# Performance work log

Hardware: AMD Instinct MI355X
Metric: run time of the kernel (lower is better)

The kernel has to match this reference:

```python
import jax, jax.numpy as jnp
import numpy as np

OFR = 2.0      # offset_range_factor
WSIZE = 8      # window_size
SPLIT = 1      # split_size


def _grid_sample(img, grid):
    # torch.nn.functional.grid_sample: bilinear, align_corners=True, padding_mode='zeros'
    # img: (B,C,H,W); grid: (B,Gh,Gw,2) with (x,y) in [-1,1]
    B, C, H, W = img.shape
    gx = (grid[..., 0] + 1.0) * 0.5 * (W - 1)
    gy = (grid[..., 1] + 1.0) * 0.5 * (H - 1)
    x0 = jnp.floor(gx)
    y0 = jnp.floor(gy)
    wx1 = gx - x0
    wy1 = gy - y0
    imgf = img.reshape(B, C, H * W)

    def corner(yc, xc, wgt):
        valid = (xc >= 0) & (xc <= W - 1) & (yc >= 0) & (yc <= H - 1)
        idx = (jnp.clip(yc, 0, H - 1) * W + jnp.clip(xc, 0, W - 1)).astype(jnp.int32)
        g = jnp.take_along_axis(imgf, idx.reshape(B, 1, -1), axis=2)  # (B,C,N)
        return g * (wgt * valid).reshape(B, 1, -1)

    out = (corner(y0, x0, (1 - wy1) * (1 - wx1)) + corner(y0, x0 + 1, (1 - wy1) * wx1)
           + corner(y0 + 1, x0, wy1 * (1 - wx1)) + corner(y0 + 1, x0 + 1, wy1 * wx1))
    return out.reshape(B, C, *grid.shape[1:-1])


def _win_attn(xqv, dh, dw):
    # 'b (qv c) (h dh) (w dw) -> qv (b h w) (dh dw) c' ; dot attention ; inverse rearrange
    B, cc, H, W = xqv.shape
    c = cc // 2
    t = xqv.reshape(B, 2, c, H // dh, dh, W // dw, dw)
    t = t.transpose(1, 0, 3, 5, 4, 6, 2).reshape(2, -1, dh * dw, c)
    q, v = t[0], t[1]
    atn = jax.nn.softmax(q @ jnp.swapaxes(q, -1, -2), axis=-1)
    o = atn @ v  # (nw, dh*dw, c)
    o = o.reshape(B, H // dh, W // dw, dh, dw, c).transpose(0, 5, 1, 3, 2, 4).reshape(B, c, H, W)
    return o


def setup_inputs() -> dict:
    key = jax.random.key(0)
    ks = jax.random.split(key, 16)
    C, B, H, W = 48, 2, 64, 64
    rn = lambda k, s, sc=0.05: (jax.random.normal(k, s) * sc).astype(jnp.float32)
    return {
        'x': jax.random.normal(ks[0], (B, C, H, W), jnp.float32),
        'Wq': rn(ks[1], (C, C)), 'bq': rn(ks[2], (C,)),
        'off_dw_w': rn(ks[3], (C, 1, 3, 3)), 'off_dw_b': rn(ks[4], (C,)),
        'off_ln_g': jnp.ones((C,), jnp.float32), 'off_ln_b': jnp.zeros((C,), jnp.float32),
        'off_pw_w': rn(ks[5], (2, C)),
        'Wk': rn(ks[6], (C, C)), 'bk': rn(ks[7], (C,)),
        'Wv': rn(ks[8], (C, C)), 'bv': rn(ks[9], (C,)),
        'inp_w': rn(ks[10], (2 * C, C)), 'inp_b': rn(ks[11], (2 * C,)),
        'bn_g': jnp.ones((2 * C,), jnp.float32), 'bn_b': jnp.zeros((2 * C,), jnp.float32),
        'bn_mean': jnp.zeros((2 * C,), jnp.float32), 'bn_var': jnp.ones((2 * C,), jnp.float32),
        'pout_w': rn(ks[12], (C, C)), 'pout_b': rn(ks[13], (C,)),
        'rpe': rn(ks[14], (1, 191, 191), 0.01),  # 96*2-1
    }


def reference(x, Wq, bq, off_dw_w, off_dw_b, off_ln_g, off_ln_b, off_pw_w, Wk, bk, Wv, bv,
              inp_w, inp_b, bn_g, bn_b, bn_mean, bn_var, pout_w, pout_b, rpe):
    B, C, h, w = x.shape
    scale = C ** (-0.5)
    c1 = lambda t, W_, b_=None: jnp.einsum('oc,bchw->bohw', W_, t) + (0.0 if b_ is None else b_[None, :, None, None])
    q = c1(x, Wq, bq)
    # conv_offset: depthwise 3x3 -> LayerNorm over channels -> GELU -> 1x1 to 2 ch (no bias)
    t = jax.lax.conv_general_dilated(q, off_dw_w, (1, 1), ((1, 1), (1, 1)),
                                     dimension_numbers=('NCHW', 'OIHW', 'NCHW'),
                                     feature_group_count=C) + off_dw_b[None, :, None, None]
    mu = t.mean(1, keepdims=True)
    var = ((t - mu) ** 2).mean(1, keepdims=True)
    t = (t - mu) * jax.lax.rsqrt(var + 1e-5) * off_ln_g[None, :, None, None] + off_ln_b[None, :, None, None]
    t = jax.nn.gelu(t, approximate=False)
    offset = c1(t, off_pw_w)  # (B,2,h,w), channel 0 = y, 1 = x
    n = h * w
    orange = jnp.array([1.0 / (h - 1), 1.0 / (w - 1)], jnp.float32).reshape(1, 2, 1, 1)
    offset = jnp.tanh(offset) * orange * OFR
    offset = offset.transpose(0, 2, 3, 1)  # (B,h,w,2) (y,x)
    ry = jnp.linspace(0.5, h - 0.5, h) / (h - 1) * 2.0 - 1.0
    rx = jnp.linspace(0.5, w - 0.5, w) / (w - 1) * 2.0 - 1.0
    ref = jnp.stack(jnp.meshgrid(ry, rx, indexing='ij'), -1)[None]
    pos = offset + ref  # (B,h,w,2) (y,x)
    x_sampled = _grid_sample(x, pos[..., ::-1]).reshape(B, C, n)
    # project_inp: 1x1 conv -> BatchNorm2d (eval mode)
    x2 = c1(x, inp_w, inp_b)
    x2 = (x2 - bn_mean[None, :, None, None]) * jax.lax.rsqrt(bn_var + 1e-5)[None, :, None, None] \
         * bn_g[None, :, None, None] + bn_b[None, :, None, None]
    s = 2 * C // 3
    xs0, xs1, xs2 = x2[:, :s], x2[:, s:2 * s], x2[:, 2 * s:]
    # deformable global attention
    qf = q.reshape(B, C, n)
    k = jnp.einsum('oc,bcn->bon', Wk, x_sampled) + bk[None, :, None]
    v = jnp.einsum('oc,bcn->bon', Wv, x_sampled) + bv[None, :, None]
    attn = jnp.einsum('bcm,bcn->bmn', qf, k) * scale
    gy = jnp.arange(h, dtype=jnp.float32) / (h - 1) * 2.0 - 1.0
    gx = jnp.arange(w, dtype=jnp.float32) / (w - 1) * 2.0 - 1.0
    qg = jnp.stack(jnp.meshgrid(gy, gx, indexing='ij'), -1).reshape(n, 2)
    disp = (qg[None, :, None, :] - pos.reshape(B, n, 2)[:, None, :, :]) * 0.5  # (B,m,n,2) (y,x)
    rpe_img = jnp.broadcast_to(rpe[None], (B,) + rpe.shape)  # (B,1,191,191)
    attn_bias = _grid_sample(rpe_img, disp[..., ::-1]).reshape(B, n, n)
    attn = jax.nn.softmax(attn + attn_bias, axis=2)
    out_dat = jnp.einsum('bmn,bcn->bcm', attn, v).reshape(B, C, h, w)
    # windowed / column / row local attention (shifts=0)
    out = jnp.concatenate([_win_attn(xs0, WSIZE, WSIZE),
                           _win_attn(xs1, h, SPLIT),
                           _win_attn(xs2, SPLIT, w)], axis=1)
    out = c1(out, pout_w, pout_b)
    return out * 0.5 + out_dat * 0.5
```

## Files before the change

### kernel.cpp

```cpp
#include <hip/hip_runtime.h>
#include <hip/hip_bf16.h>
#include <math.h>

#define Bsz 2
#define Cch 48
#define Hh 64
#define Ww 64
#define Nn 4096

typedef __bf16 bf16;
typedef __attribute__((ext_vector_type(8))) __bf16 bf16x8;
typedef __attribute__((ext_vector_type(4))) float f32x4;

__global__ void k_conv1x1(const float* __restrict__ in, const float* __restrict__ Wt,
                          const float* __restrict__ bias, float* __restrict__ qnc,
                          bf16* __restrict__ qbf){
  int chunk = blockIdx.x & 15;
  int o = (blockIdx.x >> 4) % Cch;
  int b = blockIdx.x / (16 * Cch);
  int p = chunk * 256 + threadIdx.x;
  float acc = bias[o];
  const float* ip = in + (b * Cch) * Nn + p;
  const float* wp = Wt + o * Cch;
  #pragma unroll
  for (int c = 0; c < Cch; c++) acc += wp[c] * ip[c * Nn];
  qnc[((size_t)(b * Nn + p)) * 48 + o] = acc;
  size_t qb = ((size_t)(b * Nn + p)) * 64;
  qbf[qb + o] = (bf16)acc;
  if (o < 16) qbf[qb + 48 + o] = (bf16)0.f;
}

__global__ __launch_bounds__(256) void k_offset_pos(const float* __restrict__ qnc,
                             const float* __restrict__ dww,
                             const float* __restrict__ dwb, const float* __restrict__ lng,
                             const float* __restrict__ lnb, const float* __restrict__ pww,
                             float* __restrict__ pos){
  int wv = threadIdx.x >> 6, lane = threadIdx.x & 63;
  int idx = blockIdx.x * 4 + wv;
  int b = idx >> 12;
  int p = idx & (Nn - 1);
  int y = p >> 6, x = p & 63;
  int c = lane;
  float t = 0.f;
  if (c < 48){
    t = dwb[c];
    #pragma unroll
    for (int ky = -1; ky <= 1; ky++){
      int yy = y + ky;
      if (yy < 0 || yy >= Hh) continue;
      #pragma unroll
      for (int kx = -1; kx <= 1; kx++){
        int xx = x + kx;
        if (xx < 0 || xx >= Ww) continue;
        t = fmaf(qnc[((size_t)(b * Nn + yy * Ww + xx)) * 48 + c],
                 dww[c * 9 + (ky + 1) * 3 + (kx + 1)], t);
      }
    }
  }
  float s = t;
  #pragma unroll
  for (int m = 1; m < 64; m <<= 1) s += __shfl_xor(s, m);
  float mean = s * (1.f / 48.f);
  float d = (c < 48) ? (t - mean) : 0.f;
  float v = d * d;
  #pragma unroll
  for (int m = 1; m < 64; m <<= 1) v += __shfl_xor(v, m);
  float rstd = rsqrtf(v * (1.f / 48.f) + 1e-5f);
  float p0 = 0.f, p1 = 0.f;
  if (c < 48){
    float u = (t - mean) * rstd * lng[c] + lnb[c];
    u = 0.5f * u * (1.f + erff(u * 0.70710678118654752f));
    p0 = pww[c] * u;
    p1 = pww[48 + c] * u;
  }
  #pragma unroll
  for (int m = 1; m < 64; m <<= 1){ p0 += __shfl_xor(p0, m); p1 += __shfl_xor(p1, m); }
  if (lane == 0){
    float posy = tanhf(p0) * (2.f / 63.f) + ((0.5f + (float)y) * (2.f / 63.f) - 1.f);
    float posx = tanhf(p1) * (2.f / 63.f) + ((0.5f + (float)x) * (2.f / 63.f) - 1.f);
    pos[idx * 2 + 0] = posy;
    pos[idx * 2 + 1] = posx;
  }
}

__global__ __launch_bounds__(512) void k_samplekv(const float* __restrict__ x,
                           const float* __restrict__ pos,
                           const float* __restrict__ Wk, const float* __restrict__ bk,
                           const float* __restrict__ Wv, const float* __restrict__ bv,
                           bf16* __restrict__ kk_bf, bf16* __restrict__ vt_bf,
                           float2* __restrict__ axay){
  __shared__ float wkt[48][49];
  __shared__ float wvt[48][49];
  __shared__ float rowb[8][48];
  int tid = threadIdx.x;
  for (int f = tid; f < 2304; f += 512){
    int o = f / 48, c = f - o * 48;
    wkt[c][o] = Wk[f];
    wvt[c][o] = Wv[f];
  }
  __syncthreads();
  int wv = tid >> 6, lane = tid & 63;
  int idx = blockIdx.x * 8 + wv;
  int b = idx >> 12;
  int n = idx & (Nn - 1);
  float py = pos[idx * 2], px = pos[idx * 2 + 1];
  if (lane == 0) axay[idx] = make_float2(95.f - 47.5f * py, 95.f - 47.5f * px);
  float gx = (px + 1.f) * 0.5f * 63.f;
  float gy = (py + 1.f) * 0.5f * 63.f;
  float x0f = floorf(gx), y0f = floorf(gy);
  float wx = gx - x0f, wy = gy - y0f;
  int x0 = (int)x0f, y0 = (int)y0f, x1 = x0 + 1, y1 = y0 + 1;
  float w00 = (1.f - wy) * (1.f - wx), w01 = (1.f - wy) * wx;
  float w10 = wy * (1.f - wx),         w11 = wy * wx;
  bool vx0 = (x0 >= 0) && (x0 < Ww), vx1 = (x1 >= 0) && (x1 < Ww);
  bool vy0 = (y0 >= 0) && (y0 < Hh), vy1 = (y1 >= 0) && (y1 < Hh);
  if (!(vx0 && vy0)) w00 = 0.f;
  if (!(vx1 && vy0)) w01 = 0.f;
  if (!(vx0 && vy1)) w10 = 0.f;
  if (!(vx1 && vy1)) w11 = 0.f;
  int cx0 = min(max(x0, 0), Ww - 1), cx1 = min(max(x1, 0), Ww - 1);
  int cy0 = min(max(y0, 0), Hh - 1), cy1 = min(max(y1, 0), Hh - 1);
  int i00 = cy0 * Ww + cx0, i01 = cy0 * Ww + cx1;
  int i10 = cy1 * Ww + cx0, i11 = cy1 * Ww + cx1;
  int c = lane;
  if (c < 48){
    const float* xc = x + ((size_t)(b * Cch + c)) * Nn;
    rowb[wv][c] = w00 * xc[i00] + w01 * xc[i01] + w10 * xc[i10] + w11 * xc[i11];
  }
  int o = lane;
  if (o < 48){
    float ka = bk[o], va = bv[o];
    #pragma unroll
    for (int cc = 0; cc < 48; cc++){
      float r = rowb[wv][cc];
      ka = fmaf(wkt[cc][o], r, ka);
      va = fmaf(wvt[cc][o], r, va);
    }
    kk_bf[(size_t)idx * 64 + o] = (bf16)ka;
    vt_bf[((size_t)(b * Cch + o)) * Nn + n] = (bf16)va;
  }
  if (o < 16) kk_bf[(size_t)idx * 64 + 48 + o] = (bf16)0.f;
}

__global__ __launch_bounds__(256, 5) void k_attn_win(const bf16* __restrict__ q_bf,
                                              const bf16* __restrict__ kk_bf,
                                              const bf16* __restrict__ vt_bf,
                                              const float2* __restrict__ axay,
                                              const float* __restrict__ rpe,
                                              float* __restrict__ o_part,
                                              float* __restrict__ s_part,
                                              const float* __restrict__ x,
                                              const float* __restrict__ iw,
                                              const float* __restrict__ ib,
                                              const float* __restrict__ bng,
                                              const float* __restrict__ bnb,
                                              const float* __restrict__ bnm,
                                              const float* __restrict__ bnv,
                                              float* __restrict__ wout){
  __shared__ __align__(16) char smem[25600];
  const int tid = threadIdx.x;
  const int wid = tid >> 6, lane = tid & 63;
  const int q16 = lane >> 4, l16 = lane & 15;

  if (blockIdx.x < 1024){
    float (*g)[26] = (float(*)[26])smem;
    float* axs  = (float*)(smem + 13312);
    int*   xlos = (int*)  (smem + 13824);
    float* wy0s = (float*)(smem + 14336);
    float* wy1s = (float*)(smem + 14848);
    int*   r0s  = (int*)  (smem + 15360);
    int*   r1s  = (int*)  (smem + 15872);
    bf16 (*ps)[136] = (bf16(*)[136])(smem + 16384);

    const int b  = blockIdx.x >> 9;
    const int kp = (blockIdx.x >> 8) & 1;
    const int m0 = (blockIdx.x & 255) * 16;
    const int wn0 = wid * 32;

    const bf16* qb = q_bf + ((size_t)(b * Nn + m0 + l16)) * 64;
    bf16x8 qf0 = *(const bf16x8*)(qb + q16 * 8);
    bf16x8 qf1 = *(const bf16x8*)(qb + 32 + q16 * 8);

    const float qgy = (float)(m0 >> 6) * (2.f / 63.f) - 1.f;
    const float byq = 47.5f * qgy;
    const float scale = 0.14433756729740643f;
    const float bx0 = 47.5f * ((float)(m0 & 63) * (2.f / 63.f) - 1.f);
    float bxr[4];
    #pragma unroll
    for (int r = 0; r < 4; r++){
      int mcol = (m0 & 63) + q16 * 4 + r;
      bxr[r] = 47.5f * ((float)mcol * (2.f / 63.f) - 1.f);
    }

    f32x4 oacc[3];
    #pragma unroll
    for (int ct = 0; ct < 3; ct++) oacc[ct] = (f32x4){0.f, 0.f, 0.f, 0.f};
    float s_runw[4] = {0.f, 0.f, 0.f, 0.f};

    for (int chk = 0; chk < 16; chk++){
      const int n0 = kp * 2048 + chk * 128;
      if (lane < 32){
        int n = wn0 + lane;
        float2 aa = axay[(size_t)b * Nn + n0 + n];
        float gyr = aa.x + byq;
        float y0f = floorf(gyr);
        float wy = gyr - y0f;
        int y0 = (int)y0f, y1 = y0 + 1;
        wy0s[n] = ((unsigned)y0 < 191u) ? (1.f - wy) : 0.f;
        wy1s[n] = ((unsigned)y1 < 191u) ? wy : 0.f;
        r0s[n] = min(max(y0, 0), 190) * 191;
        r1s[n] = min(max(y1, 0), 190) * 191;
        axs[n] = aa.y;
        xlos[n] = (int)floorf(aa.y + bx0);
      }
      {
        int s = lane >> 5, jj = lane & 31;
        if (jj < 26){
          #pragma unroll
          for (int it = 0; it < 16; it++){
            int n = wn0 + it * 2 + s;
            int xg = xlos[n] + jj;
            int cx = min(max(xg, 0), 190);
            float val = wy0s[n] * rpe[r0s[n] + cx] + wy1s[n] * rpe[r1s[n] + cx];
            g[n][jj] = ((unsigned)xg < 191u) ? val : 0.f;
          }
        }
      }
      f32x4 s0 = (f32x4){0.f, 0.f, 0.f, 0.f};
      f32x4 s1 = (f32x4){0.f, 0.f, 0.f, 0.f};
      {
        const bf16* kg = kk_bf + (size_t)(b * Nn + n0 + wn0 + l16) * 64;
        bf16x8 b00 = *(const bf16x8*)(kg + q16 * 8);
        bf16x8 b01 = *(const bf16x8*)(kg + 32 + q16 * 8);
        bf16x8 b10 = *(const bf16x8*)(kg + 16 * 64 + q16 * 8);
        bf16x8 b11 = *(const bf16x8*)(kg + 16 * 64 + 32 + q16 * 8);
        s0 = __builtin_amdgcn_mfma_f32_16x16x32_bf16(qf0, b00, s0, 0, 0, 0);
        s0 = __builtin_amdgcn_mfma_f32_16x16x32_bf16(qf1, b01, s0, 0, 0, 0);
        s1 = __builtin_amdgcn_mfma_f32_16x16x32_bf16(qf0, b10, s1, 0, 0, 0);
        s1 = __builtin_amdgcn_mfma_f32_16x16x32_bf16(qf1, b11, s1, 0, 0, 0);
      }
      #pragma unroll
      for (int nt = 0; nt < 2; nt++){
        int nl = wn0 + nt * 16 + l16;
        float ax = axs[nl];
        int xb = xlos[nl];
        f32x4 sv = nt ? s1 : s0;
        #pragma unroll
        for (int r = 0; r < 4; r++){
          float gxr = ax + bxr[r];
          float x0f = floorf(gxr);
          float wx = gxr - x0f;
          int j0 = (int)x0f - xb;
          float g0 = g[nl][j0], g1 = g[nl][j0 + 1];
          float bias = fmaf(wx, g1 - g0, g0);
          float e = __expf(fmaf(sv[r], scale, bias));
          s_runw[r] += e;
          ps[q16 * 4 + r][nl] = (bf16)e;
        }
      }
      {
        bf16x8 pa = *(const bf16x8*)&ps[l16][wn0 + q16 * 8];
        const bf16* vgb = vt_bf + (size_t)(b * Cch + l16) * Nn + n0 + wn0 + q16 * 8;
        #pragma unroll
        for (int ct = 0; ct < 3; ct++){
          bf16x8 vb = *(const bf16x8*)(vgb + (size_t)(ct * 16) * Nn);
          oacc[ct] = __builtin_amdgcn_mfma_f32_16x16x32_bf16(pa, vb, oacc[ct], 0, 0, 0);
        }
      }
    }
    #pragma unroll
    for (int r = 0; r < 4; r++){
      #pragma unroll
      for (int msk = 1; msk < 16; msk <<= 1)
        s_runw[r] += __shfl_xor(s_runw[r], msk);
    }
    __syncthreads();
    float* ored = (float*)g;
    float* sred = axs;
    #pragma unroll
    for (int ct = 0; ct < 3; ct++)
      #pragma unroll
      for (int r = 0; r < 4; r++)
        ored[(wid * 16 + q16 * 4 + r) * 48 + ct * 16 + l16] = oacc[ct][r];
    if (l16 == 0){
      #pragma unroll
      for (int r = 0; r < 4; r++) sred[wid * 16 + q16 * 4 + r] = s_runw[r];
    }
    __syncthreads();
    size_t obase = ((size_t)(b * 2 + kp) * Cch) * Nn;
    #pragma unroll
    for (int e = 0; e < 3; e++){
      int idx = tid + e * 256;
      int c = idx >> 4, mm = idx & 15;
      float v = ored[mm * 48 + c] + ored[(16 + mm) * 48 + c]
              + ored[(32 + mm) * 48 + c] + ored[(48 + mm) * 48 + c];
      o_part[obase + (size_t)c * Nn + m0 + mm] = v;
    }
    if (tid < 16)
      s_part[(size_t)(b * 2 + kp) * Nn + m0 + tid] =
          sred[tid] + sred[16 + tid] + sred[32 + tid] + sred[48 + tid];
  } else {
    bf16 (*xs)[72]  = (bf16(*)[72])smem;
    bf16 (*wtt)[72] = (bf16(*)[72])(smem + 9216);
    bf16 (*qs)[72]  = (bf16(*)[72])(smem + 13824);
    bf16 (*vst)[72] = (bf16(*)[72])(smem + 23040);
    float* bnsc = (float*)(smem + 25344);
    float* bnsh = (float*)(smem + 25472);
    bf16 (*psw)[72] = xs;

    int wb = blockIdx.x - 1024;
    int s = wb >> 7;
    int r7 = wb & 127;
    int b = r7 >> 6, wi = r7 & 63;
    for (int f = tid; f < 64 * 48; f += 256){
      int t = f & 63, c = f >> 6;
      int p = (s == 0) ? (((wi >> 3) * 8 + (t >> 3)) * 64 + (wi & 7) * 8 + (t & 7))
            : (s == 1) ? (t * 64 + wi) : (wi * 64 + t);
      xs[t][c] = (bf16)x[((size_t)(b * 48 + c)) * Nn + p];
    }
    for (int f = tid; f < 64 * 16; f += 256){
      int t = f >> 4, j = f & 15;
      xs[t][48 + j] = (bf16)0.f;
      qs[t][16 + j] = (bf16)0.f;
    }
    for (int f = tid; f < 32 * 64; f += 256){
      int o = f >> 6, c = f & 63;
      wtt[o][c] = (c < 48) ? (bf16)iw[(s * 32 + o) * 48 + c] : (bf16)0.f;
    }
    if (tid < 32){
      int ch = s * 32 + tid;
      float sc = bng[ch] * rsqrtf(bnv[ch] + 1e-5f);
      bnsc[tid] = sc;
      bnsh[tid] = (ib[ch] - bnm[ch]) * sc + bnb[ch];
    }
    __syncthreads();
    {
      bf16x8 a0 = *(const bf16x8*)&xs[wid * 16 + l16][q16 * 8];
      bf16x8 a1 = *(const bf16x8*)&xs[wid * 16 + l16][32 + q16 * 8];
      #pragma unroll
      for (int nt = 0; nt < 2; nt++){
        bf16x8 b0 = *(const bf16x8*)&wtt[nt * 16 + l16][q16 * 8];
        bf16x8 b1 = *(const bf16x8*)&wtt[nt * 16 + l16][32 + q16 * 8];
        f32x4 acc = (f32x4){0.f, 0.f, 0.f, 0.f};
        acc = __builtin_amdgcn_mfma_f32_16x16x32_bf16(a0, b0, acc, 0, 0, 0);
        acc = __builtin_amdgcn_mfma_f32_16x16x32_bf16(a1, b1, acc, 0, 0, 0);
        float scv = bnsc[nt * 16 + l16], shv = bnsh[nt * 16 + l16];
        #pragma unroll
        for (int r = 0; r < 4; r++){
          float v = fmaf(acc[r], scv, shv);
          int tok = wid * 16 + q16 * 4 + r;
          if (nt == 0) qs[tok][l16] = (bf16)v;
          else         vst[l16][tok] = (bf16)v;
        }
      }
    }
    __syncthreads();
    f32x4 sreg[4];
    {
      bf16x8 aq = *(const bf16x8*)&qs[wid * 16 + l16][q16 * 8];
      #pragma unroll
      for (int nt = 0; nt < 4; nt++){
        bf16x8 bq = *(const bf16x8*)&qs[nt * 16 + l16][q16 * 8];
        f32x4 acc = (f32x4){0.f, 0.f, 0.f, 0.f};
        sreg[nt] = __builtin_amdgcn_mfma_f32_16x16x32_bf16(aq, bq, acc, 0, 0, 0);
      }
    }
    float rinv[4];
    #pragma unroll
    for (int r = 0; r < 4; r++){
      float mx = fmaxf(fmaxf(sreg[0][r], sreg[1][r]), fmaxf(sreg[2][r], sreg[3][r]));
      #pragma unroll
      for (int msk = 1; msk < 16; msk <<= 1) mx = fmaxf(mx, __shfl_xor(mx, msk));
      float sum = 0.f;
      #pragma unroll
      for (int nt = 0; nt < 4; nt++){
        float e = __expf(sreg[nt][r] - mx);
        sum += e;
        psw[wid * 16 + q16 * 4 + r][nt * 16 + l16] = (bf16)e;
      }
      #pragma unroll
      for (int msk = 1; msk < 16; msk <<= 1) sum += __shfl_xor(sum, msk);
      rinv[r] = 1.f / sum;
    }
    f32x4 oac = (f32x4){0.f, 0.f, 0.f, 0.f};
    {
      bf16x8 pa0 = *(const bf16x8*)&psw[wid * 16 + l16][q16 * 8];
      bf16x8 pa1 = *(const bf16x8*)&psw[wid * 16 + l16][32 + q16 * 8];
      bf16x8 vb0 = *(const bf16x8*)&vst[l16][q16 * 8];
      bf16x8 vb1 = *(const bf16x8*)&vst[l16][32 + q16 * 8];
      oac = __builtin_amdgcn_mfma_f32_16x16x32_bf16(pa0, vb0, oac, 0, 0, 0);
      oac = __builtin_amdgcn_mfma_f32_16x16x32_bf16(pa1, vb1, oac, 0, 0, 0);
    }
    #pragma unroll
    for (int r = 0; r < 4; r++){
      int tok = wid * 16 + q16 * 4 + r;
      int p = (s == 0) ? (((wi >> 3) * 8 + (tok >> 3)) * 64 + (wi & 7) * 8 + (tok & 7))
            : (s == 1) ? (tok * 64 + wi) : (wi * 64 + tok);
      wout[((size_t)(b * 48 + s * 16 + l16)) * Nn + p] = oac[r] * rinv[r];
    }
  }
}

__global__ void k_final(const float* __restrict__ win, const float* __restrict__ pw,
                        const float* __restrict__ pb, const float* __restrict__ o_part,
                        const float* __restrict__ s_part, float* __restrict__ out){
  int chunk = blockIdx.x & 15;
  int o = (blockIdx.x >> 4) % Cch;
  int b = blockIdx.x / (16 * Cch);
  int p = chunk * 256 + threadIdx.x;
  float acc = pb[o];
  const float* ip = win + (b * Cch) * Nn + p;
  const float* wp = pw + o * Cch;
  #pragma unroll
  for (int c = 0; c < Cch; c++) acc += wp[c] * ip[c * Nn];
  float sden = s_part[(size_t)(b * 2) * Nn + p] + s_part[(size_t)(b * 2 + 1) * Nn + p];
  float odv = (o_part[((size_t)(b * 2) * Cch + o) * Nn + p]
             + o_part[((size_t)(b * 2 + 1) * Cch + o) * Nn + p]) / sden;
  out[(b * Cch + o) * Nn + p] = 0.5f * acc + 0.5f * odv;
}

extern "C" void kernel_launch(void* const* d_in, const int* in_sizes, int n_in,
                              void* d_out, int out_size, void* d_ws, size_t ws_size,
                              hipStream_t stream){
  const float* x   = (const float*)d_in[0];
  const float* Wq  = (const float*)d_in[1];
  const float* bq  = (const float*)d_in[2];
  const float* dww = (const float*)d_in[3];
  const float* dwb = (const float*)d_in[4];
  const float* lng = (const float*)d_in[5];
  const float* lnb = (const float*)d_in[6];
  const float* pww = (const float*)d_in[7];
  const float* Wk  = (const float*)d_in[8];
  const float* bk  = (const float*)d_in[9];
  const float* Wv  = (const float*)d_in[10];
  const float* bv  = (const float*)d_in[11];
  const float* iw  = (const float*)d_in[12];
  const float* ib  = (const float*)d_in[13];
  const float* bng = (const float*)d_in[14];
  const float* bnb = (const float*)d_in[15];
  const float* bnm = (const float*)d_in[16];
  const float* bnv = (const float*)d_in[17];
  const float* pw  = (const float*)d_in[18];
  const float* pb  = (const float*)d_in[19];
  const float* rpe = (const float*)d_in[20];

  float*  ws     = (float*)d_ws;
  float*  qnc    = ws;
  float*  o_part = ws;
  float*  pos    = ws + 786432;
  float2* axay   = (float2*)(ws + 802816);
  float*  wout   = ws + 819200;
  bf16*   q_bf   = (bf16*)(ws + 1212416);
  bf16*   kk_bf  = (bf16*)(ws + 1474560);
  bf16*   vt_bf  = (bf16*)(ws + 1736704);
  float*  s_part = ws + 1933312;
  float*  out    = (float*)d_out;

  k_conv1x1   <<<Bsz * Cch * 16, 256, 0, stream>>>(x, Wq, bq, qnc, q_bf);
  k_offset_pos<<<(Bsz * Nn) / 4, 256, 0, stream>>>(qnc, dww, dwb, lng, lnb, pww, pos);
  k_samplekv  <<<(Bsz * Nn) / 8, 512, 0, stream>>>(x, pos, Wk, bk, Wv, bv,
                                                   kk_bf, vt_bf, axay);
  k_attn_win  <<<Bsz * 512 + 384, 256, 0, stream>>>(q_bf, kk_bf, vt_bf, axay, rpe,
                                                    o_part, s_part,
                                                    x, iw, ib, bng, bnb, bnm, bnv, wout);
  k_final     <<<Bsz * Cch * 16, 256, 0, stream>>>(wout, pw, pb, o_part,
                                                   s_part, out);
}
```

Measured before the change: 199.6 us.

## Emit channel-last x copy in conv1x1 and coalesce sampling gathers and V stores

The 1x1 conv kernel is restructured so each block handles 64 pixels and computes all 48 output channels from registers. It stages results through shared memory for vectorized channel-last writes of q, the bf16 padded q, and a new channel-last copy of x. The sampling kernel then gathers bilinear corners from the channel-last x, so each wave reads contiguous 48-float rows instead of 48 strided channel planes. V transposed stores are also batched through shared memory into 8-wide bf16 vector writes. The cost is an extra workspace buffer and an extra full write of x.

New measurement: 200.8 us. No clear change (+0.6%).

```diff
diff --git a/kernel.cpp b/kernel.cpp
--- a/kernel.cpp
+++ b/kernel.cpp
@@ -12,22 +12,60 @@
 typedef __attribute__((ext_vector_type(8))) __bf16 bf16x8;
 typedef __attribute__((ext_vector_type(4))) float f32x4;
 
-__global__ void k_conv1x1(const float* __restrict__ in, const float* __restrict__ Wt,
+__global__ __launch_bounds__(256) void k_conv1x1(const float* __restrict__ x,
+                          const float* __restrict__ Wt,
                           const float* __restrict__ bias, float* __restrict__ qnc,
-                          bf16* __restrict__ qbf){
-  int chunk = blockIdx.x & 15;
-  int o = (blockIdx.x >> 4) % Cch;
-  int b = blockIdx.x / (16 * Cch);
-  int p = chunk * 256 + threadIdx.x;
-  float acc = bias[o];
-  const float* ip = in + (b * Cch) * Nn + p;
-  const float* wp = Wt + o * Cch;
-  #pragma unroll
-  for (int c = 0; c < Cch; c++) acc += wp[c] * ip[c * Nn];
-  qnc[((size_t)(b * Nn + p)) * 48 + o] = acc;
-  size_t qb = ((size_t)(b * Nn + p)) * 64;
-  qbf[qb + o] = (bf16)acc;
-  if (o < 16) qbf[qb + 48 + o] = (bf16)0.f;
+                          bf16* __restrict__ qbf, float* __restrict__ xnc){
+  __shared__ float st[64][49];
+  int tid = threadIdx.x;
+  int px = tid & 63, og = tid >> 6;
+  int P0 = blockIdx.x * 64;
+  int b = P0 >> 12;
+  int p = (P0 & (Nn - 1)) + px;
+  float xr[48];
+  #pragma unroll
+  for (int c = 0; c < 48; c++) xr[c] = x[((size_t)(b * 48 + c)) * Nn + p];
+  #pragma unroll
+  for (int j = 0; j < 12; j++) st[px][og * 12 + j] = xr[og * 12 + j];
+  __syncthreads();
+  #pragma unroll
+  for (int k = 0; k < 3; k++){
+    int g = tid + k * 256;
+    int rpx = g / 12, c4 = (g % 12) * 4;
+    *(float4*)&xnc[((size_t)(P0 + rpx)) * 48 + c4] = *(const float4*)&st[rpx][c4];
+  }
+  float acc[12];
+  #pragma unroll
+  for (int j = 0; j < 12; j++) acc[j] = bias[og * 12 + j];
+  #pragma unroll
+  for (int c = 0; c < 48; c++){
+    float xv = xr[c];
+    #pragma unroll
+    for (int j = 0; j < 12; j++)
+      acc[j] = fmaf(Wt[(og * 12 + j) * 48 + c], xv, acc[j]);
+  }
+  __syncthreads();
+  #pragma unroll
+  for (int j = 0; j < 12; j++) st[px][og * 12 + j] = acc[j];
+  __syncthreads();
+  #pragma unroll
+  for (int k = 0; k < 3; k++){
+    int g = tid + k * 256;
+    int rpx = g / 12, c4 = (g % 12) * 4;
+    *(float4*)&qnc[((size_t)(P0 + rpx)) * 48 + c4] = *(const float4*)&st[rpx][c4];
+  }
+  #pragma unroll
+  for (int k = 0; k < 2; k++){
+    int g = tid + k * 256;
+    int row = g >> 3, seg = g & 7;
+    bf16 tmp[8];
+    #pragma unroll
+    for (int e = 0; e < 8; e++){
+      int c = seg * 8 + e;
+      tmp[e] = (c < 48) ? (bf16)st[row][c] : (bf16)0.f;
+    }
+    *(bf16x8*)&qbf[((size_t)(P0 + row)) * 64 + seg * 8] = *(bf16x8*)tmp;
+  }
 }
 
 __global__ __launch_bounds__(256) void k_offset_pos(const float* __restrict__ qnc,
@@ -83,7 +121,7 @@
   }
 }
 
-__global__ __launch_bounds__(512) void k_samplekv(const float* __restrict__ x,
+__global__ __launch_bounds__(512) void k_samplekv(const float* __restrict__ xnc,
                            const float* __restrict__ pos,
                            const float* __restrict__ Wk, const float* __restrict__ bk,
                            const float* __restrict__ Wv, const float* __restrict__ bv,
@@ -92,6 +130,7 @@
   __shared__ float wkt[48][49];
   __shared__ float wvt[48][49];
   __shared__ float rowb[8][48];
+  __shared__ bf16 vst[8][48];
   int tid = threadIdx.x;
   for (int f = tid; f < 2304; f += 512){
     int o = f / 48, c = f - o * 48;
@@ -124,8 +163,11 @@
   int i10 = cy1 * Ww + cx0, i11 = cy1 * Ww + cx1;
   int c = lane;
   if (c < 48){
-    const float* xc = x + ((size_t)(b * Cch + c)) * Nn;
-    rowb[wv][c] = w00 * xc[i00] + w01 * xc[i01] + w10 * xc[i10] + w11 * xc[i11];
+    const float* r00 = xnc + ((size_t)(b * Nn + i00)) * 48;
+    const float* r01 = xnc + ((size_t)(b * Nn + i01)) * 48;
+    const float* r10 = xnc + ((size_t)(b * Nn + i10)) * 48;
+    const float* r11 = xnc + ((size_t)(b * Nn + i11)) * 48;
+    rowb[wv][c] = w00 * r00[c] + w01 * r01[c] + w10 * r10[c] + w11 * r11[c];
   }
   int o = lane;
   if (o < 48){
@@ -137,9 +179,18 @@
       va = fmaf(wvt[cc][o], r, va);
     }
     kk_bf[(size_t)idx * 64 + o] = (bf16)ka;
-    vt_bf[((size_t)(b * Cch + o)) * Nn + n] = (bf16)va;
+    vst[wv][o] = (bf16)va;
   }
   if (o < 16) kk_bf[(size_t)idx * 64 + 48 + o] = (bf16)0.f;
+  __syncthreads();
+  if (tid < 48){
+    int cc = tid;
+    int n0 = (blockIdx.x * 8) & (Nn - 1);
+    bf16 tmp[8];
+    #pragma unroll
+    for (int j = 0; j < 8; j++) tmp[j] = vst[j][cc];
+    *(bf16x8*)&vt_bf[((size_t)(b * 48 + cc)) * Nn + n0] = *(bf16x8*)tmp;
+  }
 }
 
 __global__ __launch_bounds__(256, 5) void k_attn_win(const bf16* __restrict__ q_bf,
@@ -454,11 +505,12 @@
   bf16*   kk_bf  = (bf16*)(ws + 1474560);
   bf16*   vt_bf  = (bf16*)(ws + 1736704);
   float*  s_part = ws + 1933312;
+  float*  xnc    = ws + 1949696;
   float*  out    = (float*)d_out;
 
-  k_conv1x1   <<<Bsz * Cch * 16, 256, 0, stream>>>(x, Wq, bq, qnc, q_bf);
+  k_conv1x1   <<<(Bsz * Nn) / 64, 256, 0, stream>>>(x, Wq, bq, qnc, q_bf, xnc);
   k_offset_pos<<<(Bsz * Nn) / 4, 256, 0, stream>>>(qnc, dww, dwb, lng, lnb, pww, pos);
-  k_samplekv  <<<(Bsz * Nn) / 8, 512, 0, stream>>>(x, pos, Wk, bk, Wv, bv,
+  k_samplekv  <<<(Bsz * Nn) / 8, 512, 0, stream>>>(xnc, pos, Wk, bk, Wv, bv,
                                                    kk_bf, vt_bf, axay);
   k_attn_win  <<<Bsz * 512 + 384, 256, 0, stream>>>(q_bf, kk_bf, vt_bf, axay, rpe,
                                                     o_part, s_part,
```
